# Optimization experiments

Measured on AMD Instinct MI355X. Metric: run time of the kernel, lower is better.

Reference implementation:

```python
import math
import jax, jax.numpy as jnp
import numpy as np

B, N, E, H = 1, 4096, 256, 8
D = E // H  # head dim = 32


def setup_inputs() -> dict:
    key = jax.random.key(0)
    ks = jax.random.split(key, 10)
    s = 1.0 / math.sqrt(E)
    return {
        "x": jax.random.normal(ks[0], (B, N, E), dtype=jnp.float32),
        "adjacency": jax.random.randint(ks[1], (B, N, N), 0, 2, dtype=jnp.int32),
        "Wq": jax.random.normal(ks[2], (E, E), dtype=jnp.float32) * s,
        "bq": jnp.zeros((E,), dtype=jnp.float32),
        "Wk": jax.random.normal(ks[3], (E, E), dtype=jnp.float32) * s,
        "bk": jnp.zeros((E,), dtype=jnp.float32),
        "Wv": jax.random.normal(ks[4], (E, E), dtype=jnp.float32) * s,
        "bv": jnp.zeros((E,), dtype=jnp.float32),
        "Wo": jax.random.normal(ks[5], (E, E), dtype=jnp.float32) * s,
        "bo": jnp.zeros((E,), dtype=jnp.float32),
    }


def reference(x, adjacency, Wq, bq, Wk, bk, Wv, bv, Wo, bo):
    b, n, e = x.shape
    # projections (torch Linear: x @ W.T + b), split into heads -> [B,H,N,D]
    def heads(y):
        return y.reshape(b, n, H, D).transpose(0, 2, 1, 3)
    q = heads(x @ Wq.T + bq)
    k = heads(x @ Wk.T + bk)
    v = heads(x @ Wv.T + bv)
    scores = jnp.einsum("bhnd,bhmd->bhnm", q, k) / math.sqrt(D)
    mask = (adjacency[:, None, :, :] == 0)  # [B,1,N,N]
    scores = jnp.where(mask, -jnp.inf, scores)
    w = jax.nn.softmax(scores, axis=-1)
    out = jnp.einsum("bhnm,bhmd->bhnd", w, v)
    out = out.transpose(0, 2, 1, 3).reshape(b, n, e)
    return out @ Wo.T + bo
```

## Files before the change

### kernel.cpp

```cpp
#include <hip/hip_runtime.h>
#include <math.h>


#define NTOK 4096
#define EDIM 256
#define HEADS 8
#define HD 32
#define NSPLIT 2
#define QSCALE 0.17677669529663687f
#define LOG2E 1.4426950408889634f
#define CINIT (-11.541560327111707f)

typedef __attribute__((ext_vector_type(8))) short bf16x8;
typedef __attribute__((ext_vector_type(4))) float f32x4;
typedef __attribute__((ext_vector_type(4))) unsigned long long u64x4;

static __device__ inline short f2bf(float f) {
    unsigned u = __float_as_uint(f);
    u = (u + 0x7FFFu + ((u >> 16) & 1u)) >> 16;
    return (short)u;
}
static __device__ inline bf16x8 pack8(float4 a, float4 b) {
    bf16x8 r;
    r[0] = f2bf(a.x); r[1] = f2bf(a.y); r[2] = f2bf(a.z); r[3] = f2bf(a.w);
    r[4] = f2bf(b.x); r[5] = f2bf(b.y); r[6] = f2bf(b.z); r[7] = f2bf(b.w);
    return r;
}
static __device__ inline unsigned packtrunc(float a, float b) {
    return __builtin_amdgcn_perm(__float_as_uint(b), __float_as_uint(a),
                                 0x07060302u);
}
static __device__ inline float sel_mask(float v, unsigned long long m) {
    float r;
    asm("v_cndmask_b32 %0, 0, %1, %2" : "=v"(r) : "v"(v), "s"(m));
    return r;
}

__global__ __launch_bounds__(256) void cast_w(
    const float* __restrict__ Wq, const float* __restrict__ Wk,
    const float* __restrict__ Wv, const float* __restrict__ Wo,
    short* __restrict__ wqb, short* __restrict__ wkb,
    short* __restrict__ wvb, short* __restrict__ wob)
{
    const int gid = blockIdx.x * 256 + threadIdx.x;
    const int e = gid * 4;
    const int wsel = e >> 16;
    const int off = e & 65535;
    const float* src = (wsel == 0) ? Wq : (wsel == 1) ? Wk : (wsel == 2) ? Wv : Wo;
    short* dst = (wsel == 0) ? wqb : (wsel == 1) ? wkb : (wsel == 2) ? wvb : wob;
    float4 v = *(const float4*)&src[off];
    uint2 t;
    t.x = (unsigned short)f2bf(v.x) | ((unsigned)(unsigned short)f2bf(v.y) << 16);
    t.y = (unsigned short)f2bf(v.z) | ((unsigned)(unsigned short)f2bf(v.w) << 16);
    *(uint2*)&dst[off] = t;
}

__global__ __launch_bounds__(256) void prep_qkv(
    const int* __restrict__ adj, unsigned long long* __restrict__ maskT,
    const float* __restrict__ x,
    const short* __restrict__ Wqb, const short* __restrict__ Wkb,
    const short* __restrict__ Wvb,
    const float* __restrict__ bq, const float* __restrict__ bk,
    const float* __restrict__ bv,
    short* __restrict__ qo, short* __restrict__ ko, short* __restrict__ vto)
{
    const int bid = blockIdx.x;
    const int tid = threadIdx.x;
    if (bid < 16384) {
        const int w = bid * 4 + (tid >> 6);
        const int l = tid & 63;
        const int qb = w >> 8;
        const int kt = (w >> 2) & 63;
        const int b = w & 3;
        const int row = qb * 16 + (l & 15);
        const int col = kt * 64 + b * 16 + ((l >> 4) & 3) * 4;
        const int4 av = *(const int4*)&adj[row * NTOK + col];
        const unsigned long long m0 = __ballot(av.x != 0);
        const unsigned long long m1 = __ballot(av.y != 0);
        const unsigned long long m2 = __ballot(av.z != 0);
        const unsigned long long m3 = __ballot(av.w != 0);
        if (l == 0) {
            unsigned long long* dst = &maskT[(size_t)w * 4];
            dst[0] = m0; dst[1] = m1; dst[2] = m2; dst[3] = m3;
        }
    } else {
        const int bid2 = bid - 16384;
        const int wv = tid >> 6, lane = tid & 63;
        const int grp = lane >> 4, lcol = lane & 15;
        const int y = bid2 >> 6;
        const int wsel = y >> 2;
        const int n0 = (y & 3) << 6;
        const int m0 = (bid2 & 63) * 64 + wv * 16;
        const short* __restrict__ W = (wsel == 0) ? Wqb : (wsel == 1) ? Wkb : Wvb;
        const float* __restrict__ bias = (wsel == 0) ? bq : (wsel == 1) ? bk : bv;

        bf16x8 af[8];
#pragma unroll
        for (int k = 0; k < 8; ++k) {
            const float* p = &x[(m0 + lcol) * 256 + k * 32 + grp * 8];
            af[k] = pack8(*(const float4*)p, *(const float4*)(p + 4));
        }

        f32x4 acc[4] = {};
#pragma unroll
        for (int k = 0; k < 8; ++k) {
#pragma unroll
            for (int t = 0; t < 4; ++t) {
                const bf16x8 bt =
                    *(const bf16x8*)&W[(n0 + t * 16 + lcol) * 256 + k * 32 + grp * 8];
                acc[t] = __builtin_amdgcn_mfma_f32_16x16x32_bf16(af[k], bt, acc[t], 0, 0, 0);
            }
        }
#pragma unroll
        for (int t = 0; t < 4; ++t) {
            const int feat = n0 + t * 16 + lcol;
            const float bval = bias[feat];
            const int h = feat >> 5, d = feat & 31;
            if (wsel == 2) {
                uint2 o;
                o.x = (unsigned short)f2bf(acc[t][0] + bval) |
                      ((unsigned)(unsigned short)f2bf(acc[t][1] + bval) << 16);
                o.y = (unsigned short)f2bf(acc[t][2] + bval) |
                      ((unsigned)(unsigned short)f2bf(acc[t][3] + bval) << 16);
                *(uint2*)&vto[h * (HD * NTOK) + d * NTOK + m0 + grp * 4] = o;
            } else {
                short* __restrict__ out = (wsel == 0) ? qo : ko;
                const float sc = (wsel == 0) ? (QSCALE * LOG2E) : 1.0f;
#pragma unroll
                for (int j = 0; j < 4; ++j)
                    out[h * (NTOK * HD) + (m0 + grp * 4 + j) * HD + d] =
                        f2bf((acc[t][j] + bval) * sc);
            }
        }
    }
}

__global__ __launch_bounds__(256) void attn_mfma(
    const short* __restrict__ qg, const short* __restrict__ kg,
    const short* __restrict__ vtg, const unsigned long long* __restrict__ maskT,
    float* __restrict__ o_part, float* __restrict__ l_part)
{
    const int h = blockIdx.y;
    const int split = blockIdx.z;
    const int q0 = blockIdx.x << 6;
    const short* __restrict__ Q  = qg  + h * (NTOK * HD);
    const short* __restrict__ K  = kg  + h * (NTOK * HD);
    const short* __restrict__ Vt = vtg + h * (HD * NTOK);

    __shared__ short Ks[2][64][40];
    __shared__ short Vs[2][32][72];
    __shared__ short P_lds[4][16][76];

    const int tid = threadIdx.x;
    const int wv = tid >> 6;
    const int lane = tid & 63;
    const int grp = lane >> 4;
    const int lcol = lane & 15;
    const int q0w = q0 + wv * 16;

    const int krow = tid >> 2, kc8 = (tid & 3) << 3;
    const int vrow = tid >> 3, vc8 = (tid & 7) << 3;

    const bf16x8 qfrag = *(const bf16x8*)&Q[(q0w + lcol) * HD + grp * 8];

    const int qb = __builtin_amdgcn_readfirstlane(blockIdx.x * 4 + wv);
    const unsigned long long* __restrict__ mbase = maskT + (size_t)qb * 1024;

    f32x4 ot[2] = {};
    float lsum = 0.f;

    const int kt_begin = split * (64 / NSPLIT);
    const int kt_end = kt_begin + (64 / NSPLIT);

    {
        const int k0 = kt_begin << 6;
        const int4 kr = *(const int4*)&K[(k0 + krow) * HD + kc8];
        const int4 vr = *(const int4*)&Vt[vrow * NTOK + k0 + vc8];
        *(int4*)&Ks[0][krow][kc8] = kr;
        *(int4*)&Vs[0][vrow][vc8] = vr;
    }
    __syncthreads();

    int cur = 0;
    for (int kt = kt_begin; kt < kt_end; ++kt) {
        int4 kr, vr;
        const bool has_next = (kt + 1 < kt_end);
        if (has_next) {
            const int k0n = (kt + 1) << 6;
            kr = *(const int4*)&K[(k0n + krow) * HD + kc8];
            vr = *(const int4*)&Vt[vrow * NTOK + k0n + vc8];
        }

        const u64x4* mp = (const u64x4*)(mbase + kt * 16);
        const u64x4 wa = mp[0], wb = mp[1], wc = mp[2], wd = mp[3];

        bf16x8 kf[4], vf[4];
#pragma unroll
        for (int b = 0; b < 4; ++b)
            kf[b] = *(const bf16x8*)&Ks[cur][b * 16 + lcol][grp * 8];
#pragma unroll
        for (int c = 0; c < 2; ++c) {
            vf[c * 2 + 0] = *(const bf16x8*)&Vs[cur][c * 16 + lcol][grp * 8];
            vf[c * 2 + 1] = *(const bf16x8*)&Vs[cur][c * 16 + lcol][32 + grp * 8];
        }

        f32x4 s[4];
#pragma unroll
        for (int b = 0; b < 4; ++b)
            s[b] = __builtin_amdgcn_mfma_f32_16x16x32_bf16(
                kf[b], qfrag, (f32x4){CINIT, CINIT, CINIT, CINIT}, 0, 0, 0);

#pragma unroll
        for (int b = 0; b < 4; ++b) {
            const u64x4 wj = (b == 0) ? wa : (b == 1) ? wb : (b == 2) ? wc : wd;
            const float p0 = sel_mask(__builtin_amdgcn_exp2f(s[b][0]), wj[0]);
            const float p1 = sel_mask(__builtin_amdgcn_exp2f(s[b][1]), wj[1]);
            const float p2 = sel_mask(__builtin_amdgcn_exp2f(s[b][2]), wj[2]);
            const float p3 = sel_mask(__builtin_amdgcn_exp2f(s[b][3]), wj[3]);
            lsum += (p0 + p1) + (p2 + p3);
            uint2 t;
            t.x = packtrunc(p0, p1);
            t.y = packtrunc(p2, p3);
            *(uint2*)&P_lds[wv][lcol][b * 16 + grp * 4] = t;
        }

        const uint2 pl0 = *(const uint2*)&P_lds[wv][lcol][grp * 8];
        const uint2 pl1 = *(const uint2*)&P_lds[wv][lcol][grp * 8 + 4];
        const uint2 pl2 = *(const uint2*)&P_lds[wv][lcol][32 + grp * 8];
        const uint2 pl3 = *(const uint2*)&P_lds[wv][lcol][32 + grp * 8 + 4];
        struct { uint2 a, b; } u0 = {pl0, pl1}, u1 = {pl2, pl3};
        const bf16x8 pf0 = __builtin_bit_cast(bf16x8, u0);
        const bf16x8 pf1 = __builtin_bit_cast(bf16x8, u1);

#pragma unroll
        for (int c = 0; c < 2; ++c) {
            ot[c] = __builtin_amdgcn_mfma_f32_16x16x32_bf16(vf[c * 2 + 0], pf0, ot[c], 0, 0, 0);
            ot[c] = __builtin_amdgcn_mfma_f32_16x16x32_bf16(vf[c * 2 + 1], pf1, ot[c], 0, 0, 0);
        }

        if (has_next) {
            *(int4*)&Ks[cur ^ 1][krow][kc8] = kr;
            *(int4*)&Vs[cur ^ 1][vrow][vc8] = vr;
        }
        __syncthreads();
        cur ^= 1;
    }

    lsum += __shfl_xor(lsum, 16);
    lsum += __shfl_xor(lsum, 32);

    float* __restrict__ ob = o_part + split * (NTOK * EDIM);
#pragma unroll
    for (int c = 0; c < 2; ++c) {
        float4 st;
        st.x = ot[c][0]; st.y = ot[c][1]; st.z = ot[c][2]; st.w = ot[c][3];
        *(float4*)&ob[(q0w + lcol) * EDIM + h * HD + c * 16 + grp * 4] = st;
    }
    if (grp == 0)
        l_part[split * (NTOK * HEADS) + (q0w + lcol) * HEADS + h] = lsum;
}

__global__ __launch_bounds__(256) void out_mfma(
    const float* __restrict__ o_part, const float* __restrict__ l_part,
    const short* __restrict__ Wob, const float* __restrict__ bo,
    float* __restrict__ Y)
{
    const int tid = threadIdx.x;
    const int wv = tid >> 6, lane = tid & 63;
    const int grp = lane >> 4, lcol = lane & 15;
    const int n0 = blockIdx.y << 6;
    const int m0 = blockIdx.x * 64 + wv * 16;
    const int r = m0 + lcol;

    bf16x8 af[8];
#pragma unroll
    for (int k = 0; k < 8; ++k) {
        float4 s0 = {0.f, 0.f, 0.f, 0.f}, s1 = {0.f, 0.f, 0.f, 0.f};
        float lv = 0.f;
#pragma unroll
        for (int s = 0; s < NSPLIT; ++s) {
            const float* op = &o_part[s * (NTOK * EDIM) + r * EDIM + k * 32 + grp * 8];
            const float4 t0 = *(const float4*)op;
            const float4 t1 = *(const float4*)(op + 4);
            s0.x += t0.x; s0.y += t0.y; s0.z += t0.z; s0.w += t0.w;
            s1.x += t1.x; s1.y += t1.y; s1.z += t1.z; s1.w += t1.w;
            lv += l_part[s * (NTOK * HEADS) + r * HEADS + k];
        }
        const float inv = 1.0f / lv;
        s0.x *= inv; s0.y *= inv; s0.z *= inv; s0.w *= inv;
        s1.x *= inv; s1.y *= inv; s1.z *= inv; s1.w *= inv;
        af[k] = pack8(s0, s1);
    }

    f32x4 acc[4] = {};
#pragma unroll
    for (int k = 0; k < 8; ++k) {
#pragma unroll
        for (int t = 0; t < 4; ++t) {
            const bf16x8 bt =
                *(const bf16x8*)&Wob[(n0 + t * 16 + lcol) * 256 + k * 32 + grp * 8];
            acc[t] = __builtin_amdgcn_mfma_f32_16x16x32_bf16(af[k], bt, acc[t], 0, 0, 0);
        }
    }
#pragma unroll
    for (int t = 0; t < 4; ++t) {
        const float bval = bo[n0 + t * 16 + lcol];
#pragma unroll
        for (int j = 0; j < 4; ++j)
            Y[(m0 + grp * 4 + j) * EDIM + n0 + t * 16 + lcol] = acc[t][j] + bval;
    }
}

extern "C" void kernel_launch(void* const* d_in, const int* in_sizes, int n_in,
                              void* d_out, int out_size, void* d_ws, size_t ws_size,
                              hipStream_t stream) {
    (void)in_sizes; (void)n_in; (void)out_size; (void)ws_size;
    const float* x  = (const float*)d_in[0];
    const int*  adj = (const int*)d_in[1];
    const float* Wq = (const float*)d_in[2];
    const float* bq = (const float*)d_in[3];
    const float* Wk = (const float*)d_in[4];
    const float* bk = (const float*)d_in[5];
    const float* Wv = (const float*)d_in[6];
    const float* bv = (const float*)d_in[7];
    const float* Wo = (const float*)d_in[8];
    const float* bo = (const float*)d_in[9];

    char* ws = (char*)d_ws;
    short* q_ws  = (short*)(ws);
    short* k_ws  = (short*)(ws + (2u << 20));
    short* vt_ws = (short*)(ws + (4u << 20));
    unsigned long long* maskT =
        (unsigned long long*)(ws + (6u << 20));
    short* Wq_bf = (short*)(ws + (8u << 20));
    short* Wk_bf = Wq_bf + (EDIM * EDIM);
    short* Wv_bf = Wk_bf + (EDIM * EDIM);
    short* Wo_bf = Wv_bf + (EDIM * EDIM);
    float* l_part = (float*)(ws + (9u << 20));
    float* o_part = (float*)(ws + (12u << 20));

    cast_w<<<dim3(256), 256, 0, stream>>>(Wq, Wk, Wv, Wo,
                                          Wq_bf, Wk_bf, Wv_bf, Wo_bf);
    prep_qkv<<<dim3(16384 + 768), 256, 0, stream>>>(
        adj, maskT, x, Wq_bf, Wk_bf, Wv_bf, bq, bk, bv, q_ws, k_ws, vt_ws);
    attn_mfma<<<dim3(64, HEADS, NSPLIT), 256, 0, stream>>>(
        q_ws, k_ws, vt_ws, maskT, o_part, l_part);
    out_mfma<<<dim3(64, 4), 256, 0, stream>>>(o_part, l_part, Wo_bf, bo,
                                              (float*)d_out);
}
```

Baseline: 186.6 us.

## Fold weight cast into prep kernel and batch mask packing per wave

Removes the separate cast_w launch. The QKV projection now reads fp32 weights directly and converts them to bf16 in registers, and the Wo cast moves into extra blocks of prep_qkv. Mask packing now has each wave handle four 64-column tiles with four independent adjacency loads, cutting the mask grid from 16384 to 4096 blocks. The costs are redundant weight conversion in every projection block and double the weight bytes read, traded against one fewer launch and more memory-level parallelism in the dominant adjacency scan.

```diff
diff --git a/kernel.cpp b/kernel.cpp
--- a/kernel.cpp
+++ b/kernel.cpp
@@ -36,62 +36,26 @@
     return r;
 }
 
-__global__ __launch_bounds__(256) void cast_w(
-    const float* __restrict__ Wq, const float* __restrict__ Wk,
-    const float* __restrict__ Wv, const float* __restrict__ Wo,
-    short* __restrict__ wqb, short* __restrict__ wkb,
-    short* __restrict__ wvb, short* __restrict__ wob)
-{
-    const int gid = blockIdx.x * 256 + threadIdx.x;
-    const int e = gid * 4;
-    const int wsel = e >> 16;
-    const int off = e & 65535;
-    const float* src = (wsel == 0) ? Wq : (wsel == 1) ? Wk : (wsel == 2) ? Wv : Wo;
-    short* dst = (wsel == 0) ? wqb : (wsel == 1) ? wkb : (wsel == 2) ? wvb : wob;
-    float4 v = *(const float4*)&src[off];
-    uint2 t;
-    t.x = (unsigned short)f2bf(v.x) | ((unsigned)(unsigned short)f2bf(v.y) << 16);
-    t.y = (unsigned short)f2bf(v.z) | ((unsigned)(unsigned short)f2bf(v.w) << 16);
-    *(uint2*)&dst[off] = t;
-}
-
 __global__ __launch_bounds__(256) void prep_qkv(
     const int* __restrict__ adj, unsigned long long* __restrict__ maskT,
     const float* __restrict__ x,
-    const short* __restrict__ Wqb, const short* __restrict__ Wkb,
-    const short* __restrict__ Wvb,
+    const float* __restrict__ Wq, const float* __restrict__ Wk,
+    const float* __restrict__ Wv, const float* __restrict__ Wo,
     const float* __restrict__ bq, const float* __restrict__ bk,
     const float* __restrict__ bv,
-    short* __restrict__ qo, short* __restrict__ ko, short* __restrict__ vto)
+    short* __restrict__ qo, short* __restrict__ ko, short* __restrict__ vto,
+    short* __restrict__ wob)
 {
     const int bid = blockIdx.x;
     const int tid = threadIdx.x;
-    if (bid < 16384) {
-        const int w = bid * 4 + (tid >> 6);
-        const int l = tid & 63;
-        const int qb = w >> 8;
-        const int kt = (w >> 2) & 63;
-        const int b = w & 3;
-        const int row = qb * 16 + (l & 15);
-        const int col = kt * 64 + b * 16 + ((l >> 4) & 3) * 4;
-        const int4 av = *(const int4*)&adj[row * NTOK + col];
-        const unsigned long long m0 = __ballot(av.x != 0);
-        const unsigned long long m1 = __ballot(av.y != 0);
-        const unsigned long long m2 = __ballot(av.z != 0);
-        const unsigned long long m3 = __ballot(av.w != 0);
-        if (l == 0) {
-            unsigned long long* dst = &maskT[(size_t)w * 4];
-            dst[0] = m0; dst[1] = m1; dst[2] = m2; dst[3] = m3;
-        }
-    } else {
-        const int bid2 = bid - 16384;
+    if (bid < 768) {
         const int wv = tid >> 6, lane = tid & 63;
         const int grp = lane >> 4, lcol = lane & 15;
-        const int y = bid2 >> 6;
+        const int y = bid >> 6;
         const int wsel = y >> 2;
         const int n0 = (y & 3) << 6;
-        const int m0 = (bid2 & 63) * 64 + wv * 16;
-        const short* __restrict__ W = (wsel == 0) ? Wqb : (wsel == 1) ? Wkb : Wvb;
+        const int m0 = (bid & 63) * 64 + wv * 16;
+        const float* __restrict__ W = (wsel == 0) ? Wq : (wsel == 1) ? Wk : Wv;
         const float* __restrict__ bias = (wsel == 0) ? bq : (wsel == 1) ? bk : bv;
 
         bf16x8 af[8];
@@ -106,8 +70,8 @@
         for (int k = 0; k < 8; ++k) {
 #pragma unroll
             for (int t = 0; t < 4; ++t) {
-                const bf16x8 bt =
-                    *(const bf16x8*)&W[(n0 + t * 16 + lcol) * 256 + k * 32 + grp * 8];
+                const float* p = &W[(n0 + t * 16 + lcol) * 256 + k * 32 + grp * 8];
+                const bf16x8 bt = pack8(*(const float4*)p, *(const float4*)(p + 4));
                 acc[t] = __builtin_amdgcn_mfma_f32_16x16x32_bf16(af[k], bt, acc[t], 0, 0, 0);
             }
         }
@@ -132,6 +96,41 @@
                         f2bf((acc[t][j] + bval) * sc);
             }
         }
+    } else if (bid < 768 + 4096) {
+        const int u = (bid - 768) * 4 + (tid >> 6);
+        const int l = tid & 63;
+        const int qb = u >> 6;
+        const int rem = u & 63;
+        const int b = rem >> 4;
+        const int ktq = rem & 15;
+        const int row = qb * 16 + (l & 15);
+        const int colb = b * 16 + ((l >> 4) & 3) * 4;
+        const int* __restrict__ rp = &adj[row * NTOK + colb];
+        const int4 a0 = *(const int4*)(rp + (ktq * 4 + 0) * 64);
+        const int4 a1 = *(const int4*)(rp + (ktq * 4 + 1) * 64);
+        const int4 a2 = *(const int4*)(rp + (ktq * 4 + 2) * 64);
+        const int4 a3 = *(const int4*)(rp + (ktq * 4 + 3) * 64);
+#pragma unroll
+        for (int i = 0; i < 4; ++i) {
+            const int4 av = (i == 0) ? a0 : (i == 1) ? a1 : (i == 2) ? a2 : a3;
+            const unsigned long long m0 = __ballot(av.x != 0);
+            const unsigned long long m1 = __ballot(av.y != 0);
+            const unsigned long long m2 = __ballot(av.z != 0);
+            const unsigned long long m3 = __ballot(av.w != 0);
+            if (l == 0) {
+                unsigned long long* dst =
+                    &maskT[(size_t)qb * 1024 + (ktq * 4 + i) * 16 + b * 4];
+                dst[0] = m0; dst[1] = m1; dst[2] = m2; dst[3] = m3;
+            }
+        }
+    } else {
+        const int gid = (bid - 768 - 4096) * 256 + tid;
+        const int off = gid * 4;
+        float4 v = *(const float4*)&Wo[off];
+        uint2 t;
+        t.x = (unsigned short)f2bf(v.x) | ((unsigned)(unsigned short)f2bf(v.y) << 16);
+        t.y = (unsigned short)f2bf(v.z) | ((unsigned)(unsigned short)f2bf(v.w) << 16);
+        *(uint2*)&wob[off] = t;
     }
 }
 
@@ -287,9 +286,12 @@
             lv += l_part[s * (NTOK * HEADS) + r * HEADS + k];
         }
         const float inv = 1.0f / lv;
-        s0.x *= inv; s0.y *= inv; s0.z *= inv; s0.w *= inv;
-        s1.x *= inv; s1.y *= inv; s1.z *= inv; s1.w *= inv;
-        af[k] = pack8(s0, s1);
+        bf16x8 t;
+        t[0] = f2bf(s0.x * inv); t[1] = f2bf(s0.y * inv);
+        t[2] = f2bf(s0.z * inv); t[3] = f2bf(s0.w * inv);
+        t[4] = f2bf(s1.x * inv); t[5] = f2bf(s1.y * inv);
+        t[6] = f2bf(s1.z * inv); t[7] = f2bf(s1.w * inv);
+        af[k] = t;
     }
 
     f32x4 acc[4] = {};
@@ -332,17 +334,12 @@
     short* vt_ws = (short*)(ws + (4u << 20));
     unsigned long long* maskT =
         (unsigned long long*)(ws + (6u << 20));
-    short* Wq_bf = (short*)(ws + (8u << 20));
-    short* Wk_bf = Wq_bf + (EDIM * EDIM);
-    short* Wv_bf = Wk_bf + (EDIM * EDIM);
-    short* Wo_bf = Wv_bf + (EDIM * EDIM);
+    short* Wo_bf = (short*)(ws + (8u << 20));
     float* l_part = (float*)(ws + (9u << 20));
     float* o_part = (float*)(ws + (12u << 20));
 
-    cast_w<<<dim3(256), 256, 0, stream>>>(Wq, Wk, Wv, Wo,
-                                          Wq_bf, Wk_bf, Wv_bf, Wo_bf);
-    prep_qkv<<<dim3(16384 + 768), 256, 0, stream>>>(
-        adj, maskT, x, Wq_bf, Wk_bf, Wv_bf, bq, bk, bv, q_ws, k_ws, vt_ws);
+    prep_qkv<<<dim3(768 + 4096 + 64), 256, 0, stream>>>(
+        adj, maskT, x, Wq, Wk, Wv, Wo, bq, bk, bv, q_ws, k_ws, vt_ws, Wo_bf);
     attn_mfma<<<dim3(64, HEADS, NSPLIT), 256, 0, stream>>>(
         q_ws, k_ws, vt_ws, maskT, o_part, l_part);
     out_mfma<<<dim3(64, 4), 256, 0, stream>>>(o_part, l_part, Wo_bf, bo,
```

Result: slower. 190.7 us (+2.2%).
